# Kernel optimization log

Hardware: AMD Instinct MI355X
Metric: run time of the kernel (lower is better)

## Reference

```python
import jax, jax.numpy as jnp
import numpy as np

EMBED_DIM = 1024
NUM_HEADS = 16
HEAD_DIM = EMBED_DIM // NUM_HEADS


def setup_inputs() -> dict:
    key = jax.random.key(0)
    k1, k2, k3, k4, k5 = jax.random.split(key, 5)
    B, S, D = 1, 4096, EMBED_DIM
    scale = 0.02
    return {
        "input": jax.random.normal(k1, (B, S, D), dtype=jnp.float32),
        "Wqkv": jax.random.normal(k2, (D, 3 * D), dtype=jnp.float32) * scale,
        "bqkv": jax.random.normal(k3, (3 * D,), dtype=jnp.float32) * scale,
        "Wo": jax.random.normal(k4, (D, D), dtype=jnp.float32) * scale,
        "bo": jax.random.normal(k5, (D,), dtype=jnp.float32) * scale,
    }


def reference(input, Wqkv, bqkv, Wo, bo):
    B, S, D = input.shape
    H, Hd = NUM_HEADS, HEAD_DIM
    qkv = input @ Wqkv + bqkv                        # [B, S, 3D]
    qkv = qkv.reshape(B, S, 3, H, Hd)
    qkv = jnp.transpose(qkv, (2, 0, 3, 1, 4))        # [3, B, H, S, Hd]
    q, k, v = qkv[0], qkv[1], qkv[2]
    scores = jnp.einsum("bhsd,bhtd->bhst", q, k) / (Hd ** 0.5)  # [B,H,S,S]
    causal = jnp.tril(jnp.ones((S, S), dtype=bool))[None, None]
    scores = jnp.where(causal, scores, -jnp.inf)
    attn = jax.nn.softmax(scores, axis=-1)
    out = jnp.einsum("bhst,bhtd->bhsd", attn, v)     # [B,H,S,Hd]
    out = jnp.transpose(out, (0, 2, 1, 3)).reshape(B, S, D)
    return out @ Wo + bo
```

## Files before the change

kernel.cpp:

```cpp
#include <hip/hip_runtime.h>

typedef __bf16 bf16;
typedef __bf16 bf16x8 __attribute__((ext_vector_type(8)));
typedef float f32x4 __attribute__((ext_vector_type(4)));
typedef float f32x16 __attribute__((ext_vector_type(16)));

#define MFMA16(a, b, c) __builtin_amdgcn_mfma_f32_16x16x32_bf16((a), (b), (c), 0, 0, 0)
#define MFMA32(a, b, c) __builtin_amdgcn_mfma_f32_32x32x16_bf16((a), (b), (c), 0, 0, 0)

typedef const __attribute__((address_space(1))) uint32_t glb_u32;
typedef __attribute__((address_space(3))) uint32_t lds_u32;
#define GLOAD16(gp, lp) __builtin_amdgcn_global_load_lds((glb_u32*)(gp), (lds_u32*)(lp), 16, 0, 0)

__global__ __launch_bounds__(256) void k_convX(const float* __restrict__ in, bf16* __restrict__ out) {
    size_t i = ((size_t)blockIdx.x * 256 + threadIdx.x) * 8;
    float4 a = *(const float4*)(in + i);
    float4 b = *(const float4*)(in + i + 4);
    bf16 e[8];
    e[0] = (bf16)a.x; e[1] = (bf16)a.y; e[2] = (bf16)a.z; e[3] = (bf16)a.w;
    e[4] = (bf16)b.x; e[5] = (bf16)b.y; e[6] = (bf16)b.z; e[7] = (bf16)b.w;
    uint4 u; __builtin_memcpy(&u, e, 16);
    *(uint4*)(out + i) = u;
}

__global__ __launch_bounds__(256) void k_tconv(const float* __restrict__ in, bf16* __restrict__ out,
                                               int R, int C) {
    __shared__ float tile[64][65];
    int bx = blockIdx.x, by = blockIdx.y;
    int t = threadIdx.x;
    for (int i = 0; i < 16; ++i) {
        int e = i * 256 + t; int r = e >> 6, c = e & 63;
        tile[r][c] = in[(size_t)(by * 64 + r) * C + bx * 64 + c];
    }
    __syncthreads();
    for (int i = 0; i < 16; ++i) {
        int e = i * 256 + t; int r = e >> 6, c = e & 63;
        out[(size_t)(bx * 64 + r) * R + by * 64 + c] = (bf16)tile[c][r];
    }
}

__global__ __launch_bounds__(256) void k_kpack(const uint4* __restrict__ in, uint4* __restrict__ out) {
    int c = blockIdx.x * 256 + threadIdx.x;
    int h = c >> 15;
    int r = c & 32767;
    int tile = r >> 8, kst = (r >> 6) & 3, l = r & 63;
    int t = tile * 32 + (l & 31);
    int dc = kst * 2 + (l >> 5);
    out[c] = in[((size_t)h * 4096 + t) * 8 + dc];
}

__global__ __launch_bounds__(256) void k_vtrans(const bf16* __restrict__ V, uint4* __restrict__ Vfr) {
    __shared__ bf16 tl[64][68];
    int t0 = blockIdx.x * 64;
    int h = blockIdx.y;
    int t = threadIdx.x;
    const bf16* Vh = V + (size_t)h * 4096 * 64;
    #pragma unroll
    for (int i = 0; i < 2; ++i) {
        int c = i * 256 + t; int row = c >> 3, ch = c & 7;
        uint4 v = *(const uint4*)(Vh + (size_t)(t0 + row) * 64 + ch * 8);
        bf16 e[8]; __builtin_memcpy(e, &v, 16);
        #pragma unroll
        for (int j = 0; j < 8; ++j) tl[row][ch * 8 + j] = e[j];
    }
    __syncthreads();
    uint4* Vfh = Vfr + (size_t)h * 32768;
    #pragma unroll
    for (int i = 0; i < 2; ++i) {
        int c = i * 256 + t; int d = c >> 3, tch = c & 7;
        bf16 e[8];
        #pragma unroll
        for (int j = 0; j < 8; ++j) e[j] = tl[tch * 8 + j][d];
        uint4 u; __builtin_memcpy(&u, e, 16);
        int tile = blockIdx.x * 2 + (tch >> 2);
        int chunk = tile * 256 + ((d >> 5) * 2 + ((tch >> 1) & 1)) * 64 + (d & 31) + 32 * (tch & 1);
        Vfh[chunk] = u;
    }
}

__device__ __forceinline__ void gemm128_core(const bf16* __restrict__ A, const bf16* __restrict__ Bt,
                                             int r0, int c0, int Kd, char* As, char* Bs,
                                             f32x4 (&acc)[4][4]) {
    int t = threadIdx.x, l = t & 63, w = t >> 6;
    int g = l >> 4, li = l & 15;
    int wr = w >> 1, wc = w & 1;
    for (int k0 = 0; k0 < Kd; k0 += 64) {
        __syncthreads();
        #pragma unroll
        for (int i = 0; i < 4; ++i) {
            int slot = i * 256 + t;
            int row = slot >> 3;
            int ch  = (slot & 7) ^ (row & 7);
            int base = (i * 256 + w * 64) * 16;
            GLOAD16(A  + (size_t)(r0 + row) * Kd + k0 + ch * 8, As + base);
            GLOAD16(Bt + (size_t)(c0 + row) * Kd + k0 + ch * 8, Bs + base);
        }
        __syncthreads();
        __builtin_amdgcn_s_setprio(1);
        #pragma unroll
        for (int kk = 0; kk < 2; ++kk) {
            bf16x8 af[4], bfr[4];
            #pragma unroll
            for (int m = 0; m < 4; ++m) {
                int row = wr * 64 + m * 16 + li;
                af[m] = *(const bf16x8*)(As + ((row * 128 + kk * 64 + g * 16) ^ ((row & 7) << 4)));
            }
            #pragma unroll
            for (int n = 0; n < 4; ++n) {
                int row = wc * 64 + n * 16 + li;
                bfr[n] = *(const bf16x8*)(Bs + ((row * 128 + kk * 64 + g * 16) ^ ((row & 7) << 4)));
            }
            #pragma unroll
            for (int m = 0; m < 4; ++m)
                #pragma unroll
                for (int n = 0; n < 4; ++n)
                    acc[m][n] = MFMA16(af[m], bfr[n], acc[m][n]);
        }
        __builtin_amdgcn_s_setprio(0);
    }
}

__global__ __launch_bounds__(256) void k_gemm_qkv(const bf16* __restrict__ Xb, const bf16* __restrict__ WqkvT,
                                                  const float* __restrict__ bqkv,
                                                  bf16* __restrict__ Q, bf16* __restrict__ K,
                                                  bf16* __restrict__ V) {
    __shared__ __align__(16) char As[16384];
    __shared__ __align__(16) char Bs[16384];
    int r0 = blockIdx.y * 128, c0 = blockIdx.x * 128;
    f32x4 acc[4][4] = {};
    gemm128_core(Xb, WqkvT, r0, c0, 1024, As, Bs, acc);
    int t = threadIdx.x, l = t & 63, w = t >> 6;
    int g = l >> 4, li = l & 15;
    int wr = w >> 1, wc = w & 1;
    int colbase = c0 + wc * 64;
    int sec = colbase >> 10;
    int head = (colbase & 1023) >> 6;
    bf16* dst = (sec == 0) ? Q : (sec == 1) ? K : V;
    float scale = (sec == 0) ? 0.125f * 1.44269504f : 1.0f;
    #pragma unroll
    for (int m = 0; m < 4; ++m)
        #pragma unroll
        for (int n = 0; n < 4; ++n) {
            int hd = n * 16 + li;
            float bias = bqkv[colbase + hd];
            #pragma unroll
            for (int r = 0; r < 4; ++r) {
                int row = r0 + wr * 64 + m * 16 + g * 4 + r;
                dst[(size_t)(head * 4096 + row) * 64 + hd] = (bf16)((acc[m][n][r] + bias) * scale);
            }
        }
}

__global__ __launch_bounds__(256) void k_gemm_out(const bf16* __restrict__ Ob, const bf16* __restrict__ WoT,
                                                  const float* __restrict__ bo, float* __restrict__ out) {
    __shared__ __align__(16) char As[16384];
    __shared__ __align__(16) char Bs[16384];
    int r0 = blockIdx.y * 128, c0 = blockIdx.x * 128;
    f32x4 acc[4][4] = {};
    gemm128_core(Ob, WoT, r0, c0, 1024, As, Bs, acc);
    int t = threadIdx.x, l = t & 63, w = t >> 6;
    int g = l >> 4, li = l & 15;
    int wr = w >> 1, wc = w & 1;
    #pragma unroll
    for (int m = 0; m < 4; ++m)
        #pragma unroll
        for (int n = 0; n < 4; ++n) {
            int col = c0 + wc * 64 + n * 16 + li;
            float bias = bo[col];
            #pragma unroll
            for (int r = 0; r < 4; ++r) {
                int row = r0 + wr * 64 + m * 16 + g * 4 + r;
                out[(size_t)row * 1024 + col] = acc[m][n][r] + bias;
            }
        }
}

__device__ __forceinline__ unsigned pkbf(float a, float b) {
    bf16 h0 = (bf16)a, h1 = (bf16)b;
    unsigned short u0, u1;
    __builtin_memcpy(&u0, &h0, 2); __builtin_memcpy(&u1, &h1, 2);
    return (unsigned)u0 | ((unsigned)u1 << 16);
}

__global__ __launch_bounds__(128) void k_attn(const bf16* __restrict__ Q, const uint4* __restrict__ Kfr,
                                              const uint4* __restrict__ Vfr, bf16* __restrict__ O) {
    __shared__ float Op[2][32][64];
    __shared__ float Ml[2][2][32];
    int bid = blockIdx.x;
    int h = bid & 15;
    int p = bid >> 4;
    int w = threadIdx.x >> 6;
    int l = threadIdx.x & 63;
    int lc = l & 31, hi = l >> 5;
    int hi4 = hi * 4, hi8 = hi * 8;
    const bf16* Qh = Q + (size_t)h * 4096 * 64;
    const uint4* Kh = Kfr + (size_t)h * 32768;
    const uint4* Vh = Vfr + (size_t)h * 32768;
    int jA = p, jB = 127 - p;
    int ntA = jA + 1, ntB = jB + 1;
    int hA = ntA >> 1, hB = ntB >> 1;
    int j1 = w ? jA : jB, b1 = w ? hA : hB, e1 = w ? ntA : ntB;
    int j2 = w ? jB : jA, e2 = w ? hB : hA;

    f32x16 oacc[2];
    float m, lsum;
    uint4 kA[4], vA[4], kB[4], vB[4];
    bf16x8 qf[4];

    auto compute = [&](int jj, int tt, uint4 (&kf)[4], uint4 (&vf)[4]) {
        f32x16 sacc = {};
        #pragma unroll
        for (int kst = 0; kst < 4; ++kst) {
            bf16x8 kk; __builtin_memcpy(&kk, &kf[kst], 16);
            sacc = MFMA32(kk, qf[kst], sacc);
        }
        if (tt == jj) {
            #pragma unroll
            for (int r = 0; r < 16; ++r) {
                int tloc = (r & 3) + 8 * (r >> 2) + hi4;
                if (tloc > lc) sacc[r] = -1e30f;
            }
        }
        float t8[8];
        #pragma unroll
        for (int r = 0; r < 8; ++r) t8[r] = fmaxf(sacc[r], sacc[r + 8]);
        float t4a = fmaxf(fmaxf(t8[0], t8[1]), fmaxf(t8[2], t8[3]));
        float t4b = fmaxf(fmaxf(t8[4], t8[5]), fmaxf(t8[6], t8[7]));
        float pm = fmaxf(t4a, t4b);
        pm = fmaxf(pm, __shfl_xor(pm, 32));
        if (!__all(pm - m <= 8.0f)) {
            float mn = fmaxf(m, pm);
            float al = exp2f(m - mn);
            #pragma unroll
            for (int r = 0; r < 16; ++r) {
                int ql = (r & 3) + 8 * (r >> 2) + hi4;
                float alb = __shfl(al, ql);
                oacc[0][r] *= alb;
                oacc[1][r] *= alb;
            }
            lsum *= al;
            m = mn;
        }
        float pv[16];
        float rs = 0.f;
        #pragma unroll
        for (int r = 0; r < 16; ++r) { pv[r] = exp2f(sacc[r] - m); rs += pv[r]; }
        lsum += rs;
        #pragma unroll
        for (int ks = 0; ks < 2; ++ks) {
            int b = ks * 8;
            unsigned a0 = pkbf(pv[b + 0], pv[b + 1]), b0 = pkbf(pv[b + 4], pv[b + 5]);
            unsigned a1 = pkbf(pv[b + 2], pv[b + 3]), b1v = pkbf(pv[b + 6], pv[b + 7]);
            unsigned xa0 = (unsigned)__shfl_xor((int)a0, 32);
            unsigned xb0 = (unsigned)__shfl_xor((int)b0, 32);
            unsigned xa1 = (unsigned)__shfl_xor((int)a1, 32);
            unsigned xb1 = (unsigned)__shfl_xor((int)b1v, 32);
            unsigned wsq[4];
            wsq[0] = hi ? xb0 : a0;
            wsq[1] = hi ? xb1 : a1;
            wsq[2] = hi ? b0 : xa0;
            wsq[3] = hi ? b1v : xa1;
            bf16x8 pa; __builtin_memcpy(&pa, wsq, 16);
            #pragma unroll
            for (int jt = 0; jt < 2; ++jt) {
                bf16x8 vv; __builtin_memcpy(&vv, &vf[jt * 2 + ks], 16);
                oacc[jt] = MFMA32(pa, vv, oacc[jt]);
            }
        }
    };

    auto runphase = [&](int jj, int tb, int te) {
        int n = te - tb;
        if (n <= 0) return;
        #pragma unroll
        for (int i = 0; i < 4; ++i) {
            kA[i] = Kh[(size_t)tb * 256 + i * 64 + l];
            vA[i] = Vh[(size_t)tb * 256 + i * 64 + l];
        }
        int i = tb;
        for (; i + 2 <= te; i += 2) {
            const uint4* Kn = Kh + (size_t)(i + 1) * 256;
            const uint4* Vn = Vh + (size_t)(i + 1) * 256;
            #pragma unroll
            for (int q = 0; q < 4; ++q) { kB[q] = Kn[q * 64 + l]; vB[q] = Vn[q * 64 + l]; }
            compute(jj, i, kA, vA);
            if (i + 2 < te) {
                const uint4* K2 = Kh + (size_t)(i + 2) * 256;
                const uint4* V2 = Vh + (size_t)(i + 2) * 256;
                #pragma unroll
                for (int q = 0; q < 4; ++q) { kA[q] = K2[q * 64 + l]; vA[q] = V2[q * 64 + l]; }
            }
            compute(jj, i + 1, kB, vB);
        }
        if (n & 1) compute(jj, te - 1, kA, vA);
    };

    #pragma unroll
    for (int kst = 0; kst < 4; ++kst)
        qf[kst] = *(const bf16x8*)(Qh + (size_t)(j1 * 32 + lc) * 64 + kst * 16 + hi8);
    m = -1e30f; lsum = 0.f;
    #pragma unroll
    for (int r = 0; r < 16; ++r) { oacc[0][r] = 0.f; oacc[1][r] = 0.f; }
    runphase(j1, b1, e1);
    lsum += __shfl_xor(lsum, 32);
    #pragma unroll
    for (int r = 0; r < 16; ++r) {
        int ql = (r & 3) + 8 * (r >> 2) + hi4;
        Op[w][ql][lc]      = oacc[0][r];
        Op[w][ql][32 + lc] = oacc[1][r];
    }
    if (hi == 0) { Ml[w][0][lc] = m; Ml[w][1][lc] = lsum; }

    #pragma unroll
    for (int kst = 0; kst < 4; ++kst)
        qf[kst] = *(const bf16x8*)(Qh + (size_t)(j2 * 32 + lc) * 64 + kst * 16 + hi8);
    m = -1e30f; lsum = 0.f;
    #pragma unroll
    for (int r = 0; r < 16; ++r) { oacc[0][r] = 0.f; oacc[1][r] = 0.f; }
    runphase(j2, 0, e2);
    lsum += __shfl_xor(lsum, 32);

    __syncthreads();

    int o = w ^ 1;
    float mo = Ml[o][0][lc], lo = Ml[o][1][lc];
    float mm = fmaxf(m, mo);
    float alr = exp2f(m - mm), alo = exp2f(mo - mm);
    float lf = lsum * alr + lo * alo;
    float inv = 1.0f / lf;
    float fr = alr * inv, fo = alo * inv;
    int q0 = j2 * 32;
    #pragma unroll
    for (int r = 0; r < 16; ++r) {
        int ql = (r & 3) + 8 * (r >> 2) + hi4;
        float frb = __shfl(fr, ql), fob = __shfl(fo, ql);
        float o0 = oacc[0][r] * frb + Op[o][ql][lc]      * fob;
        float o1 = oacc[1][r] * frb + Op[o][ql][32 + lc] * fob;
        int row = q0 + ql;
        O[(size_t)row * 1024 + h * 64 + lc]      = (bf16)o0;
        O[(size_t)row * 1024 + h * 64 + 32 + lc] = (bf16)o1;
    }
}

extern "C" void kernel_launch(void* const* d_in, const int* in_sizes, int n_in,
                              void* d_out, int out_size, void* d_ws, size_t ws_size,
                              hipStream_t stream) {
    const float* X    = (const float*)d_in[0];
    const float* Wqkv = (const float*)d_in[1];
    const float* bqkv = (const float*)d_in[2];
    const float* Wo   = (const float*)d_in[3];
    const float* bo   = (const float*)d_in[4];
    float* out = (float*)d_out;

    char* ws = (char*)d_ws;
    const size_t MB = 1024 * 1024;
    bf16*  Xb    = (bf16*)(ws);
    bf16*  WqkvT = (bf16*)(ws + 8  * MB);
    bf16*  WoT   = (bf16*)(ws + 14 * MB);
    bf16*  Qb    = (bf16*)(ws + 16 * MB);
    bf16*  Kb    = (bf16*)(ws + 24 * MB);
    bf16*  Vb    = (bf16*)(ws + 32 * MB);
    uint4* Kfr   = (uint4*)(ws + 40 * MB);
    uint4* Vfr   = (uint4*)(ws + 48 * MB);
    bf16*  Ob    = Xb;

    k_convX<<<2048, 256, 0, stream>>>(X, Xb);
    k_tconv<<<dim3(48, 16), 256, 0, stream>>>(Wqkv, WqkvT, 1024, 3072);
    k_tconv<<<dim3(16, 16), 256, 0, stream>>>(Wo, WoT, 1024, 1024);
    k_gemm_qkv<<<dim3(24, 32), 256, 0, stream>>>(Xb, WqkvT, bqkv, Qb, Kb, Vb);
    k_kpack<<<2048, 256, 0, stream>>>((const uint4*)Kb, Kfr);
    k_vtrans<<<dim3(64, 16), 256, 0, stream>>>(Vb, Vfr);
    k_attn<<<1024, 128, 0, stream>>>(Qb, Kfr, Vfr, Ob);
    k_gemm_out<<<dim3(8, 32), 256, 0, stream>>>(Ob, WoT, bo, out);
}
```

Measured before the change: 163.2 us.

## Give each attention block one query tile split across two waves

Before, each attention block handled a pair of query tiles (p and 127-p), with the two waves splitting key tiles across both phases. Now each block handles a single query tile, and its two waves each process half of that tile's key range before merging through shared memory. The grid doubles to 2048 blocks, shared memory per block halves, and launch bounds now request 4 blocks per CU, aiming for more occupancy and latency hiding. Block order runs from the smallest tile to the largest, then from the largest back down, so cost varies widely per block and load balance now depends on the hardware scheduler. The whole second wave also sits idle during the final merge.

```diff
diff --git a/kernel.cpp b/kernel.cpp
--- a/kernel.cpp
+++ b/kernel.cpp
@@ -182,13 +182,14 @@
     return (unsigned)u0 | ((unsigned)u1 << 16);
 }
 
-__global__ __launch_bounds__(128) void k_attn(const bf16* __restrict__ Q, const uint4* __restrict__ Kfr,
-                                              const uint4* __restrict__ Vfr, bf16* __restrict__ O) {
-    __shared__ float Op[2][32][64];
-    __shared__ float Ml[2][2][32];
+__global__ __launch_bounds__(128, 4) void k_attn(const bf16* __restrict__ Q, const uint4* __restrict__ Kfr,
+                                                 const uint4* __restrict__ Vfr, bf16* __restrict__ O) {
+    __shared__ float Op[32][64];
+    __shared__ float Ml[2][32];
     int bid = blockIdx.x;
     int h = bid & 15;
-    int p = bid >> 4;
+    int u = bid >> 4;
+    int jj = (u < 64) ? u : 191 - u;
     int w = threadIdx.x >> 6;
     int l = threadIdx.x & 63;
     int lc = l & 31, hi = l >> 5;
@@ -196,18 +197,20 @@
     const bf16* Qh = Q + (size_t)h * 4096 * 64;
     const uint4* Kh = Kfr + (size_t)h * 32768;
     const uint4* Vh = Vfr + (size_t)h * 32768;
-    int jA = p, jB = 127 - p;
-    int ntA = jA + 1, ntB = jB + 1;
-    int hA = ntA >> 1, hB = ntB >> 1;
-    int j1 = w ? jA : jB, b1 = w ? hA : hB, e1 = w ? ntA : ntB;
-    int j2 = w ? jB : jA, e2 = w ? hB : hA;
-
-    f32x16 oacc[2];
-    float m, lsum;
+    int nt = jj + 1;
+    int hA = (nt + 1) >> 1;
+    int tb = w ? hA : 0;
+    int te = w ? nt : hA;
+
+    f32x16 oacc[2] = {};
+    float m = -1e30f, lsum = 0.f;
     uint4 kA[4], vA[4], kB[4], vB[4];
     bf16x8 qf[4];
-
-    auto compute = [&](int jj, int tt, uint4 (&kf)[4], uint4 (&vf)[4]) {
+    #pragma unroll
+    for (int kst = 0; kst < 4; ++kst)
+        qf[kst] = *(const bf16x8*)(Qh + (size_t)(jj * 32 + lc) * 64 + kst * 16 + hi8);
+
+    auto compute = [&](int tt, uint4 (&kf)[4], uint4 (&vf)[4]) {
         f32x16 sacc = {};
         #pragma unroll
         for (int kst = 0; kst < 4; ++kst) {
@@ -269,9 +272,7 @@
         }
     };
 
-    auto runphase = [&](int jj, int tb, int te) {
-        int n = te - tb;
-        if (n <= 0) return;
+    if (te > tb) {
         #pragma unroll
         for (int i = 0; i < 4; ++i) {
             kA[i] = Kh[(size_t)tb * 256 + i * 64 + l];
@@ -283,62 +284,47 @@
             const uint4* Vn = Vh + (size_t)(i + 1) * 256;
             #pragma unroll
             for (int q = 0; q < 4; ++q) { kB[q] = Kn[q * 64 + l]; vB[q] = Vn[q * 64 + l]; }
-            compute(jj, i, kA, vA);
+            compute(i, kA, vA);
             if (i + 2 < te) {
                 const uint4* K2 = Kh + (size_t)(i + 2) * 256;
                 const uint4* V2 = Vh + (size_t)(i + 2) * 256;
                 #pragma unroll
                 for (int q = 0; q < 4; ++q) { kA[q] = K2[q * 64 + l]; vA[q] = V2[q * 64 + l]; }
             }
-            compute(jj, i + 1, kB, vB);
-        }
-        if (n & 1) compute(jj, te - 1, kA, vA);
-    };
-
-    #pragma unroll
-    for (int kst = 0; kst < 4; ++kst)
-        qf[kst] = *(const bf16x8*)(Qh + (size_t)(j1 * 32 + lc) * 64 + kst * 16 + hi8);
-    m = -1e30f; lsum = 0.f;
-    #pragma unroll
-    for (int r = 0; r < 16; ++r) { oacc[0][r] = 0.f; oacc[1][r] = 0.f; }
-    runphase(j1, b1, e1);
+            compute(i + 1, kB, vB);
+        }
+        if ((te - tb) & 1) compute(te - 1, kA, vA);
+    }
     lsum += __shfl_xor(lsum, 32);
-    #pragma unroll
-    for (int r = 0; r < 16; ++r) {
-        int ql = (r & 3) + 8 * (r >> 2) + hi4;
-        Op[w][ql][lc]      = oacc[0][r];
-        Op[w][ql][32 + lc] = oacc[1][r];
-    }
-    if (hi == 0) { Ml[w][0][lc] = m; Ml[w][1][lc] = lsum; }
-
-    #pragma unroll
-    for (int kst = 0; kst < 4; ++kst)
-        qf[kst] = *(const bf16x8*)(Qh + (size_t)(j2 * 32 + lc) * 64 + kst * 16 + hi8);
-    m = -1e30f; lsum = 0.f;
-    #pragma unroll
-    for (int r = 0; r < 16; ++r) { oacc[0][r] = 0.f; oacc[1][r] = 0.f; }
-    runphase(j2, 0, e2);
-    lsum += __shfl_xor(lsum, 32);
-
+
+    if (w == 1) {
+        #pragma unroll
+        for (int r = 0; r < 16; ++r) {
+            int ql = (r & 3) + 8 * (r >> 2) + hi4;
+            Op[ql][lc]      = oacc[0][r];
+            Op[ql][32 + lc] = oacc[1][r];
+        }
+        if (hi == 0) { Ml[0][lc] = m; Ml[1][lc] = lsum; }
+    }
     __syncthreads();
-
-    int o = w ^ 1;
-    float mo = Ml[o][0][lc], lo = Ml[o][1][lc];
-    float mm = fmaxf(m, mo);
-    float alr = exp2f(m - mm), alo = exp2f(mo - mm);
-    float lf = lsum * alr + lo * alo;
-    float inv = 1.0f / lf;
-    float fr = alr * inv, fo = alo * inv;
-    int q0 = j2 * 32;
-    #pragma unroll
-    for (int r = 0; r < 16; ++r) {
-        int ql = (r & 3) + 8 * (r >> 2) + hi4;
-        float frb = __shfl(fr, ql), fob = __shfl(fo, ql);
-        float o0 = oacc[0][r] * frb + Op[o][ql][lc]      * fob;
-        float o1 = oacc[1][r] * frb + Op[o][ql][32 + lc] * fob;
-        int row = q0 + ql;
-        O[(size_t)row * 1024 + h * 64 + lc]      = (bf16)o0;
-        O[(size_t)row * 1024 + h * 64 + 32 + lc] = (bf16)o1;
+    if (w == 0) {
+        float mo = Ml[0][lc], lo = Ml[1][lc];
+        float mm = fmaxf(m, mo);
+        float alr = exp2f(m - mm), alo = exp2f(mo - mm);
+        float lf = lsum * alr + lo * alo;
+        float inv = 1.0f / lf;
+        float fr = alr * inv, fo = alo * inv;
+        int q0 = jj * 32;
+        #pragma unroll
+        for (int r = 0; r < 16; ++r) {
+            int ql = (r & 3) + 8 * (r >> 2) + hi4;
+            float frb = __shfl(fr, ql), fob = __shfl(fo, ql);
+            float o0 = oacc[0][r] * frb + Op[ql][lc]      * fob;
+            float o1 = oacc[1][r] * frb + Op[ql][32 + lc] * fob;
+            int row = q0 + ql;
+            O[(size_t)row * 1024 + h * 64 + lc]      = (bf16)o0;
+            O[(size_t)row * 1024 + h * 64 + 32 + lc] = (bf16)o1;
+        }
     }
 }
 
@@ -370,6 +356,6 @@
     k_gemm_qkv<<<dim3(24, 32), 256, 0, stream>>>(Xb, WqkvT, bqkv, Qb, Kb, Vb);
     k_kpack<<<2048, 256, 0, stream>>>((const uint4*)Kb, Kfr);
     k_vtrans<<<dim3(64, 16), 256, 0, stream>>>(Vb, Vfr);
-    k_attn<<<1024, 128, 0, stream>>>(Qb, Kfr, Vfr, Ob);
+    k_attn<<<2048, 128, 0, stream>>>(Qb, Kfr, Vfr, Ob);
     k_gemm_out<<<dim3(8, 32), 256, 0, stream>>>(Ob, WoT, bo, out);
 }
```

Result: slower. 292.3 us (+79.1%).
